# Performance work log

Hardware: AMD Instinct MI355X
Metric: run time of the kernel (lower is better)

The kernel has to match this reference:

```python
import jax, jax.numpy as jnp
import numpy as np

B, C, L = 4, 256, 4096
NUM_GROUPS = 32
EPS = 1e-6


def setup_inputs() -> dict:
    key = jax.random.key(0)
    ks = jax.random.split(key, 8)
    s = 1.0 / np.sqrt(C)  # conv1x1 init scale
    return {
        "x": jax.random.normal(ks[0], (B, C, L), dtype=jnp.float32),
        "norm_g": jnp.ones((C,), dtype=jnp.float32),
        "norm_b": jnp.zeros((C,), dtype=jnp.float32),
        "q_w": jax.random.normal(ks[1], (C, C), dtype=jnp.float32) * s,
        "q_b": jnp.zeros((C,), dtype=jnp.float32),
        "k_w": jax.random.normal(ks[2], (C, C), dtype=jnp.float32) * s,
        "k_b": jnp.zeros((C,), dtype=jnp.float32),
        "v_w": jax.random.normal(ks[3], (C, C), dtype=jnp.float32) * s,
        "v_b": jnp.zeros((C,), dtype=jnp.float32),
        "proj_w": jax.random.normal(ks[4], (C, C), dtype=jnp.float32) * s,
        "proj_b": jnp.zeros((C,), dtype=jnp.float32),
    }


def _group_norm(x, g, b):
    # x: [B, C, L] -> groups of C//NUM_GROUPS channels
    Bx, Cx, Lx = x.shape
    xg = x.reshape(Bx, NUM_GROUPS, Cx // NUM_GROUPS, Lx)
    mean = jnp.mean(xg, axis=(2, 3), keepdims=True)
    var = jnp.var(xg, axis=(2, 3), keepdims=True)
    xn = ((xg - mean) * jax.lax.rsqrt(var + EPS)).reshape(Bx, Cx, Lx)
    return xn * g[None, :, None] + b[None, :, None]


def _conv1x1(w, b, h):
    # w: [Cout, Cin], h: [B, Cin, L]
    return jnp.einsum("oc,bcl->bol", w, h) + b[None, :, None]


def reference(x, norm_g, norm_b, q_w, q_b, k_w, k_b, v_w, v_b, proj_w, proj_b):
    h = _group_norm(x, norm_g, norm_b)
    q = _conv1x1(q_w, q_b, h)   # [B, C, L]
    k = _conv1x1(k_w, k_b, h)
    v = _conv1x1(v_w, v_b, h)

    scale = jnp.asarray(x.shape[1], x.dtype) ** -0.5
    # w_[b,i,j] = sum_c q[b,c,i] * k[b,c,j]
    w_ = jnp.einsum("bci,bcj->bij", q, k) * scale
    w_ = jax.nn.softmax(w_, axis=2)
    # h_[b,c,i] = sum_j v[b,c,j] * w_[b,i,j]
    h2 = jnp.einsum("bcj,bij->bci", v, w_)

    out = _conv1x1(proj_w, proj_b, h2)
    return x + out
```

## Files before the change

### kernel.cpp

```cpp
#include <hip/hip_runtime.h>

#define B_ 4
#define C_ 256
#define L_ 4096
#define NG 32
#define CPG 8
#define BL (B_ * L_)
#define KPART 4
#define KEYS_PP (L_ / KPART)
#define NIT (KEYS_PP / 32)
#define QLOG2E 0.09016844f

typedef __attribute__((ext_vector_type(8))) __bf16 bf16x8;
typedef __attribute__((ext_vector_type(8))) short s16x8;
typedef __attribute__((ext_vector_type(4))) float f32x4;
typedef __attribute__((ext_vector_type(16))) float f32x16;

__device__ __forceinline__ unsigned short f2bf(float f) {
  unsigned int u = __builtin_bit_cast(unsigned int, f);
  u += 0x7fffu + ((u >> 16) & 1u);
  return (unsigned short)(u >> 16);
}
__device__ __forceinline__ float bf2f(unsigned short u) {
  unsigned int v = ((unsigned int)u) << 16;
  return __builtin_bit_cast(float, v);
}
#if __has_builtin(__builtin_amdgcn_exp2f)
#define EXP2F(x) __builtin_amdgcn_exp2f(x)
#else
#define EXP2F(x) exp2f(x)
#endif

__device__ __forceinline__ void gld_lds16(const void* g, void* l) {
  __builtin_amdgcn_global_load_lds(
      (const __attribute__((address_space(1))) unsigned int*)g,
      (__attribute__((address_space(3))) unsigned int*)l, 16, 0, 0);
}

__device__ __forceinline__ float red16_add(float x) {
  int i;
  i = __builtin_amdgcn_update_dpp(0, __builtin_bit_cast(int, x), 0xB1, 0xF, 0xF, false);
  x += __builtin_bit_cast(float, i);
  i = __builtin_amdgcn_update_dpp(0, __builtin_bit_cast(int, x), 0x4E, 0xF, 0xF, false);
  x += __builtin_bit_cast(float, i);
  i = __builtin_amdgcn_update_dpp(0, __builtin_bit_cast(int, x), 0x124, 0xF, 0xF, false);
  x += __builtin_bit_cast(float, i);
  i = __builtin_amdgcn_update_dpp(0, __builtin_bit_cast(int, x), 0x128, 0xF, 0xF, false);
  x += __builtin_bit_cast(float, i);
  return x;
}

__global__ __launch_bounds__(256) void init_k(const float* __restrict__ qw,
                                              const float* __restrict__ kw,
                                              const float* __restrict__ vw,
                                              const float* __restrict__ pw,
                                              const float* __restrict__ qb,
                                              const float* __restrict__ x,
                                              unsigned short* __restrict__ wq,
                                              unsigned short* __restrict__ wk,
                                              unsigned short* __restrict__ wv,
                                              unsigned short* __restrict__ wp,
                                              float* __restrict__ qbs,
                                              float* __restrict__ stats) {
  const int bid = blockIdx.x;
  const int t = threadIdx.x;
  if (bid < 128) {
    const int m = bid >> 5;
    const int blk = bid & 31;
    const float* src = (m == 0) ? qw : (m == 1) ? kw : (m == 2) ? vw : pw;
    unsigned short* dst = (m == 0) ? wq : (m == 1) ? wk : (m == 2) ? wv : wp;
    const float sc = (m == 0) ? QLOG2E : 1.0f;
    const int base = (blk * 256 + t) * 8;
    f32x4 a = *(const f32x4*)(src + base);
    f32x4 b = *(const f32x4*)(src + base + 4);
    s16x8 o;
#pragma unroll
    for (int j = 0; j < 4; ++j) {
      o[j] = (short)f2bf(a[j] * sc);
      o[4 + j] = (short)f2bf(b[j] * sc);
    }
    *(s16x8*)(dst + base) = o;
    if (m == 0 && blk == 0) qbs[t] = qb[t] * QLOG2E;
  } else {
    const int bg = bid - 128;
    const float* base = x + (size_t)bg * (CPG * L_);
    float s = 0.f, ss = 0.f;
#pragma unroll
    for (int i = 0; i < 32; ++i) {
      f32x4 v = *(const f32x4*)(base + (size_t)(t + i * 256) * 4);
#pragma unroll
      for (int j = 0; j < 4; ++j) { s += v[j]; ss += v[j] * v[j]; }
    }
#pragma unroll
    for (int d = 1; d < 64; d <<= 1) {
      s += __shfl_xor(s, d, 64);
      ss += __shfl_xor(ss, d, 64);
    }
    __shared__ float red[8];
    if ((t & 63) == 0) { red[(t >> 6) * 2] = s; red[(t >> 6) * 2 + 1] = ss; }
    __syncthreads();
    if (t == 0) {
      float S = red[0] + red[2] + red[4] + red[6];
      float SS = red[1] + red[3] + red[5] + red[7];
      const float inv_n = 1.f / (float)(CPG * L_);
      float mean = S * inv_n;
      float var = SS * inv_n - mean * mean;
      stats[bg * 2] = mean;
      stats[bg * 2 + 1] = rsqrtf(var + 1e-6f);
    }
  }
}

__global__ __launch_bounds__(256) void gn_apply_k(const float* __restrict__ x,
                                                  const float* __restrict__ stats,
                                                  const float* __restrict__ gam,
                                                  const float* __restrict__ bet,
                                                  unsigned short* __restrict__ ht) {
  __shared__ unsigned short tile[64 * 256];
  const int blk = blockIdx.x;
  const int b = blk >> 6;
  const int l0 = (blk & 63) * 64;
  const int t = threadIdx.x;
  const int c = t;
  const float mean = stats[(b * NG + (c >> 3)) * 2];
  const float rstd = stats[(b * NG + (c >> 3)) * 2 + 1];
  const float sc = rstd * gam[c];
  const float sb = bet[c] - mean * sc;
  const float* row = x + ((size_t)(b * C_ + c)) * L_ + l0;
#pragma unroll
  for (int v = 0; v < 16; ++v) {
    f32x4 f = *(const f32x4*)(row + v * 4);
#pragma unroll
    for (int j = 0; j < 4; ++j) tile[(v * 4 + j) * 256 + c] = f2bf(f[j] * sc + sb);
  }
  __syncthreads();
#pragma unroll
  for (int i = 0; i < 8; ++i) {
    int id = t + i * 256;
    int l = id >> 5, off = id & 31;
    *(s16x8*)(ht + ((size_t)(b * L_) + l0 + l) * 256 + off * 8) =
        *(const s16x8*)(tile + l * 256 + off * 8);
  }
}

__global__ __launch_bounds__(256) void qkv_k(const unsigned short* __restrict__ ht,
                                             const unsigned short* __restrict__ wq,
                                             const unsigned short* __restrict__ wk,
                                             const unsigned short* __restrict__ wv,
                                             const float* __restrict__ qbs,
                                             const float* __restrict__ kbias,
                                             const float* __restrict__ vbias,
                                             unsigned short* __restrict__ qt,
                                             unsigned short* __restrict__ kt,
                                             unsigned short* __restrict__ vg) {
  __shared__ unsigned short Al[64 * 256];
  __shared__ unsigned short Wl[64 * 256];
  const int z = blockIdx.z;
  const unsigned short* W = (z == 0) ? wq : (z == 1) ? wk : wv;
  const float* bias = (z == 0) ? qbs : (z == 1) ? kbias : vbias;
  const int m0 = blockIdx.x * 64;
  const int n0 = blockIdx.y * 64;
  const int t = threadIdx.x;
  const int w = t >> 6, lane = t & 63, l15 = lane & 15, q = lane >> 4;
#pragma unroll
  for (int i = 0; i < 8; ++i) {
    const int seg = w * 8 + i;
    const int idx = seg * 64 + lane;
    const int row = idx >> 5, c16 = idx & 31;
    gld_lds16(ht + (size_t)(m0 + row) * 256 + ((c16 ^ (row & 7)) * 8), Al + seg * 512);
    gld_lds16(W + (size_t)(n0 + row) * 256 + ((c16 ^ (row & 7)) * 8), Wl + seg * 512);
  }
  __syncthreads();
  bf16x8 af[8];
#pragma unroll
  for (int kf = 0; kf < 8; ++kf) {
    int row = w * 16 + l15;
    af[kf] = *(const bf16x8*)(Al + row * 256 + (((kf * 4 + q) ^ (row & 7)) * 8));
  }
  f32x4 acc[4];
#pragma unroll
  for (int nf = 0; nf < 4; ++nf) {
    f32x4 cacc = {0.f, 0.f, 0.f, 0.f};
#pragma unroll
    for (int kf = 0; kf < 8; ++kf) {
      int row = nf * 16 + l15;
      bf16x8 bf = *(const bf16x8*)(Wl + row * 256 + (((kf * 4 + q) ^ (row & 7)) * 8));
      cacc = __builtin_amdgcn_mfma_f32_16x16x32_bf16(af[kf], bf, cacc, 0, 0, 0);
    }
    acc[nf] = cacc;
  }
  unsigned short* Ct = (z == 0) ? qt : kt;
#pragma unroll
  for (int nf = 0; nf < 4; ++nf) {
    const int n = n0 + nf * 16 + l15;
    const float bs = bias[n];
#pragma unroll
    for (int r = 0; r < 4; ++r) {
      const int m = m0 + w * 16 + q * 4 + r;
      const float v = acc[nf][r] + bs;
      if (z < 2) {
        Ct[(size_t)m * 256 + n] = f2bf(v);
      } else {
        const int b = m >> 12, i = m & (L_ - 1);
        const int jt = i >> 5, jj = i & 31;
        const int qc = jj >> 3, pos = jj & 7;
        vg[((size_t)(b * 128 + jt)) * 8192 + n * 32 + ((qc ^ ((n >> 1) & 3)) * 8) + pos] =
            f2bf(v);
      }
    }
  }
}

__global__ __launch_bounds__(256, 2) void attn_k(const unsigned short* __restrict__ Qt,
                                                 const unsigned short* __restrict__ Kt,
                                                 const unsigned short* __restrict__ Vg,
                                                 unsigned short* __restrict__ o0p,
                                                 unsigned short* __restrict__ o1p,
                                                 unsigned short* __restrict__ o2p,
                                                 unsigned short* __restrict__ o3p,
                                                 float* __restrict__ ml) {
  __shared__ unsigned short Kl[2][32 * 256];
  __shared__ unsigned short Vl[2][256 * 32];
  __shared__ unsigned short Pl[4 * 32 * 40];
  const int bid = blockIdx.x;
  const int g = bid & 15;
  const int b = g >> 2, part = g & 3;
  const int qi = bid >> 4;
  const int t = threadIdx.x;
  const int w = t >> 6, lane = t & 63;
  const int l15 = lane & 15, q = lane >> 4;
  const int l31 = lane & 31, h = lane >> 5;

  const int qb0 = b * L_ + qi * 128;
  const int qrow0 = qb0 + w * 32;
  bf16x8 qf[2][8];
#pragma unroll
  for (int mi = 0; mi < 2; ++mi)
#pragma unroll
    for (int kf = 0; kf < 8; ++kf)
      qf[mi][kf] =
          *(const bf16x8*)(Qt + ((size_t)(qrow0 + mi * 16 + l15)) * 256 + kf * 32 + q * 8);

  f32x16 oacc[8];
#pragma unroll
  for (int nf = 0; nf < 8; ++nf)
#pragma unroll
    for (int gg = 0; gg < 16; ++gg) oacc[nf][gg] = 0.f;
  float ls0[4] = {0.f, 0.f, 0.f, 0.f}, ls1[4] = {0.f, 0.f, 0.f, 0.f};

  const unsigned short* kbase = Kt + ((size_t)(b * L_ + part * KEYS_PP)) * 256;
  const unsigned short* vbase = Vg + ((size_t)(b * 128 + part * 32)) * 8192;
  unsigned short* Pw = Pl + w * 1280;

#pragma unroll
  for (int i = 0; i < 4; ++i) {
    const int seg = w * 4 + i;
    const int idx = seg * 64 + lane;
    const int row = idx >> 5, c16 = idx & 31;
    gld_lds16(kbase + (size_t)row * 256 + ((c16 ^ (row & 7)) * 8), &Kl[0][0] + seg * 512);
    gld_lds16(vbase + (size_t)idx * 8, &Vl[0][0] + seg * 512);
  }

  for (int it = 0; it < NIT; ++it) {
    __syncthreads();
    if (it + 1 < NIT) {
      const unsigned short* ksrc = kbase + (size_t)((it + 1) * 32) * 256;
      const unsigned short* vsrc = vbase + (size_t)(it + 1) * 8192;
      unsigned short* kd = &Kl[(it + 1) & 1][0];
      unsigned short* vd = &Vl[(it + 1) & 1][0];
#pragma unroll
      for (int i = 0; i < 4; ++i) {
        const int seg = w * 4 + i;
        const int idx = seg * 64 + lane;
        const int row = idx >> 5, c16 = idx & 31;
        gld_lds16(ksrc + (size_t)row * 256 + ((c16 ^ (row & 7)) * 8), kd + seg * 512);
        gld_lds16(vsrc + (size_t)idx * 8, vd + seg * 512);
      }
    }
    const unsigned short* Kb = &Kl[it & 1][0];
    const unsigned short* Vb = &Vl[it & 1][0];

    f32x4 s00 = {0.f, 0.f, 0.f, 0.f}, s01 = s00, s10 = s00, s11 = s00;
#pragma unroll
    for (int kf = 0; kf < 8; ++kf) {
      const int ch = ((kf * 4 + q) ^ (l15 & 7)) * 8;
      bf16x8 kb0 = *(const bf16x8*)(Kb + l15 * 256 + ch);
      bf16x8 kb1 = *(const bf16x8*)(Kb + (16 + l15) * 256 + ch);
      s00 = __builtin_amdgcn_mfma_f32_16x16x32_bf16(qf[0][kf], kb0, s00, 0, 0, 0);
      s01 = __builtin_amdgcn_mfma_f32_16x16x32_bf16(qf[0][kf], kb1, s01, 0, 0, 0);
      s10 = __builtin_amdgcn_mfma_f32_16x16x32_bf16(qf[1][kf], kb0, s10, 0, 0, 0);
      s11 = __builtin_amdgcn_mfma_f32_16x16x32_bf16(qf[1][kf], kb1, s11, 0, 0, 0);
    }
#pragma unroll
    for (int r = 0; r < 4; ++r) {
      float p00 = EXP2F(s00[r]), p01 = EXP2F(s01[r]);
      float p10 = EXP2F(s10[r]), p11 = EXP2F(s11[r]);
      ls0[r] += p00 + p01;
      ls1[r] += p10 + p11;
      Pw[(q * 4 + r) * 40 + l15] = f2bf(p00);
      Pw[(q * 4 + r) * 40 + 16 + l15] = f2bf(p01);
      Pw[(16 + q * 4 + r) * 40 + l15] = f2bf(p10);
      Pw[(16 + q * 4 + r) * 40 + 16 + l15] = f2bf(p11);
    }
    bf16x8 pa0 = *(const bf16x8*)(Pw + l31 * 40 + h * 8);
    bf16x8 pa1 = *(const bf16x8*)(Pw + l31 * 40 + 16 + h * 8);
#pragma unroll
    for (int nf = 0; nf < 8; ++nf) {
      const int c = nf * 32 + l31;
      bf16x8 v0 = *(const bf16x8*)(Vb + c * 32 + ((h ^ ((c >> 1) & 3)) * 8));
      bf16x8 v1 = *(const bf16x8*)(Vb + c * 32 + (((2 + h) ^ ((c >> 1) & 3)) * 8));
      oacc[nf] = __builtin_amdgcn_mfma_f32_32x32x16_bf16(pa0, v0, oacc[nf], 0, 0, 0);
      oacc[nf] = __builtin_amdgcn_mfma_f32_32x32x16_bf16(pa1, v1, oacc[nf], 0, 0, 0);
    }
  }

  unsigned short* opb = (part == 0) ? o0p : (part == 1) ? o1p : (part == 2) ? o2p : o3p;
#pragma unroll
  for (int nf = 0; nf < 8; ++nf)
#pragma unroll
    for (int gg = 0; gg < 16; ++gg) {
      const int row = (gg & 3) + 8 * (gg >> 2) + 4 * h;
      opb[(size_t)(qrow0 + row) * 256 + nf * 32 + l31] = f2bf(oacc[nf][gg]);
    }
#pragma unroll
  for (int r = 0; r < 4; ++r) {
    ls0[r] = red16_add(ls0[r]);
    ls1[r] = red16_add(ls1[r]);
  }
  if (l15 == 0) {
    float* mlp = ml + (size_t)part * BL;
#pragma unroll
    for (int r = 0; r < 4; ++r) {
      mlp[qrow0 + q * 4 + r] = ls0[r];
      mlp[qrow0 + 16 + q * 4 + r] = ls1[r];
    }
  }
}

__global__ __launch_bounds__(256) void merge_k(const unsigned short* __restrict__ o0p,
                                               const unsigned short* __restrict__ o1p,
                                               const unsigned short* __restrict__ o2p,
                                               const unsigned short* __restrict__ o3p,
                                               const float* __restrict__ ml,
                                               unsigned short* __restrict__ Om) {
  const int row = blockIdx.x * 8 + (threadIdx.x >> 5);
  const int c8 = threadIdx.x & 31;
  const float inv = 1.0f / (ml[row] + ml[BL + row] + ml[2 * BL + row] + ml[3 * BL + row]);
  const size_t off = (size_t)row * 256 + c8 * 8;
  s16x8 v0 = *(const s16x8*)(o0p + off);
  s16x8 v1 = *(const s16x8*)(o1p + off);
  s16x8 v2 = *(const s16x8*)(o2p + off);
  s16x8 v3 = *(const s16x8*)(o3p + off);
  s16x8 o;
#pragma unroll
  for (int j = 0; j < 8; ++j)
    o[j] = (short)f2bf((bf2f((unsigned short)v0[j]) + bf2f((unsigned short)v1[j]) +
                        bf2f((unsigned short)v2[j]) + bf2f((unsigned short)v3[j])) *
                       inv);
  *(s16x8*)(Om + off) = o;
}

__global__ __launch_bounds__(256) void proj_k(const unsigned short* __restrict__ X,
                                              const unsigned short* __restrict__ W,
                                              const float* __restrict__ bias,
                                              const float* __restrict__ xres,
                                              float* __restrict__ out) {
  __shared__ unsigned short Wl[64 * 256];
  __shared__ unsigned short Xl[64 * 256];
  const int i0 = blockIdx.x * 64;
  const int o0 = blockIdx.y * 64;
  const int b = blockIdx.z;
  const int t = threadIdx.x;
  const int w = t >> 6, lane = t & 63, l15 = lane & 15, q = lane >> 4;
#pragma unroll
  for (int i = 0; i < 8; ++i) {
    const int seg = w * 8 + i;
    const int idx = seg * 64 + lane;
    const int row = idx >> 5, c16 = idx & 31;
    gld_lds16(W + (size_t)(o0 + row) * 256 + ((c16 ^ (row & 7)) * 8), Wl + seg * 512);
    gld_lds16(X + ((size_t)(b * L_) + i0 + row) * 256 + ((c16 ^ (row & 7)) * 8),
              Xl + seg * 512);
  }
  __syncthreads();
  bf16x8 af[8];
#pragma unroll
  for (int kf = 0; kf < 8; ++kf) {
    int row = w * 16 + l15;
    af[kf] = *(const bf16x8*)(Wl + row * 256 + (((kf * 4 + q) ^ (row & 7)) * 8));
  }
  f32x4 acc[4];
#pragma unroll
  for (int nf = 0; nf < 4; ++nf) {
    f32x4 cacc = {0.f, 0.f, 0.f, 0.f};
#pragma unroll
    for (int kf = 0; kf < 8; ++kf) {
      int row = nf * 16 + l15;
      bf16x8 bf = *(const bf16x8*)(Xl + row * 256 + (((kf * 4 + q) ^ (row & 7)) * 8));
      cacc = __builtin_amdgcn_mfma_f32_16x16x32_bf16(af[kf], bf, cacc, 0, 0, 0);
    }
    acc[nf] = cacc;
  }
#pragma unroll
  for (int nf = 0; nf < 4; ++nf) {
    const int i = i0 + nf * 16 + l15;
#pragma unroll
    for (int r = 0; r < 4; ++r) {
      const int o = o0 + w * 16 + q * 4 + r;
      const size_t idx = ((size_t)(b * C_ + o)) * L_ + i;
      out[idx] = acc[nf][r] + bias[o] + xres[idx];
    }
  }
}

extern "C" void kernel_launch(void* const* d_in, const int* in_sizes, int n_in,
                              void* d_out, int out_size, void* d_ws, size_t ws_size,
                              hipStream_t stream) {
  const float* x = (const float*)d_in[0];
  const float* norm_g = (const float*)d_in[1];
  const float* norm_b = (const float*)d_in[2];
  const float* q_w = (const float*)d_in[3];
  const float* q_b = (const float*)d_in[4];
  const float* k_w = (const float*)d_in[5];
  const float* k_b = (const float*)d_in[6];
  const float* v_w = (const float*)d_in[7];
  const float* v_b = (const float*)d_in[8];
  const float* p_w = (const float*)d_in[9];
  const float* p_b = (const float*)d_in[10];
  float* out = (float*)d_out;
  (void)in_sizes; (void)n_in; (void)out_size; (void)ws_size;

  char* ws = (char*)d_ws;
  const size_t MB = 1u << 20;
  const size_t PSZ = (size_t)BL * 256 * 2;
  float* stats = (float*)ws;
  float* qbs = (float*)(ws + 1024);
  unsigned short* wq = (unsigned short*)(ws + 4096);
  unsigned short* wk = wq + 65536;
  unsigned short* wv = wk + 65536;
  unsigned short* wp = wv + 65536;
  float* ml = (float*)(ws + 640 * 1024);
  unsigned short* ht = (unsigned short*)(ws + 1 * MB);
  unsigned short* qt = (unsigned short*)(ws + 9 * MB);
  unsigned short* kt = (unsigned short*)(ws + 17 * MB);
  unsigned short* vg = (unsigned short*)(ws + 25 * MB);
  unsigned short* o0p = (unsigned short*)d_out;
  unsigned short* o1p = o0p + PSZ / 2;
  unsigned short* o2p = (unsigned short*)(ws + 33 * MB);
  unsigned short* o3p = o2p + PSZ / 2;

  init_k<<<256, 256, 0, stream>>>(q_w, k_w, v_w, p_w, q_b, x, wq, wk, wv, wp, qbs, stats);
  gn_apply_k<<<B_ * (L_ / 64), 256, 0, stream>>>(x, stats, norm_g, norm_b, ht);
  qkv_k<<<dim3((B_ * L_) / 64, C_ / 64, 3), 256, 0, stream>>>(ht, wq, wk, wv, qbs, k_b,
                                                              v_b, qt, kt, vg);
  attn_k<<<512, 256, 0, stream>>>(qt, kt, vg, o0p, o1p, o2p, o3p, ml);
  merge_k<<<BL / 8, 256, 0, stream>>>(o0p, o1p, o2p, o3p, ml, ht);
  proj_k<<<dim3(L_ / 64, C_ / 64, B_), 256, 0, stream>>>(ht, wp, p_b, x, out);
}
```

Measured before the change: 220.9 us.

## Enlarge QKV GEMM tiles and process 64-key tiles per attention iteration

The QKV projection moves to 128x128 block tiles with a two-step K loop, so each wave computes a 64x64 sub-tile with more operand reuse. The attention kernel now loads 64 keys per iteration with a new V layout grouped in 8-key chunks, and drops the K/V double buffering in favour of load-then-compute with two barriers. The P staging pitch is reduced. Global load latency in attention is no longer overlapped with compute, and the narrower P pitch may cause LDS bank conflicts or misaligned vector reads.

```diff
diff --git a/kernel.cpp b/kernel.cpp
--- a/kernel.cpp
+++ b/kernel.cpp
@@ -8,7 +8,7 @@
 #define BL (B_ * L_)
 #define KPART 4
 #define KEYS_PP (L_ / KPART)
-#define NIT (KEYS_PP / 32)
+#define NIT (KEYS_PP / 64)
 #define QLOG2E 0.09016844f
 
 typedef __attribute__((ext_vector_type(8))) __bf16 bf16x8;
@@ -143,69 +143,85 @@
   }
 }
 
-__global__ __launch_bounds__(256) void qkv_k(const unsigned short* __restrict__ ht,
-                                             const unsigned short* __restrict__ wq,
-                                             const unsigned short* __restrict__ wk,
-                                             const unsigned short* __restrict__ wv,
-                                             const float* __restrict__ qbs,
-                                             const float* __restrict__ kbias,
-                                             const float* __restrict__ vbias,
-                                             unsigned short* __restrict__ qt,
-                                             unsigned short* __restrict__ kt,
-                                             unsigned short* __restrict__ vg) {
-  __shared__ unsigned short Al[64 * 256];
-  __shared__ unsigned short Wl[64 * 256];
+__global__ __launch_bounds__(256, 2) void qkv_k(const unsigned short* __restrict__ ht,
+                                                const unsigned short* __restrict__ wq,
+                                                const unsigned short* __restrict__ wk,
+                                                const unsigned short* __restrict__ wv,
+                                                const float* __restrict__ qbs,
+                                                const float* __restrict__ kbias,
+                                                const float* __restrict__ vbias,
+                                                unsigned short* __restrict__ qt,
+                                                unsigned short* __restrict__ kt,
+                                                unsigned short* __restrict__ vg) {
+  __shared__ unsigned short Al[128 * 128];
+  __shared__ unsigned short Wl[128 * 128];
   const int z = blockIdx.z;
   const unsigned short* W = (z == 0) ? wq : (z == 1) ? wk : wv;
   const float* bias = (z == 0) ? qbs : (z == 1) ? kbias : vbias;
-  const int m0 = blockIdx.x * 64;
-  const int n0 = blockIdx.y * 64;
+  const int m0 = blockIdx.x * 128;
+  const int n0 = blockIdx.y * 128;
   const int t = threadIdx.x;
   const int w = t >> 6, lane = t & 63, l15 = lane & 15, q = lane >> 4;
-#pragma unroll
-  for (int i = 0; i < 8; ++i) {
-    const int seg = w * 8 + i;
-    const int idx = seg * 64 + lane;
-    const int row = idx >> 5, c16 = idx & 31;
-    gld_lds16(ht + (size_t)(m0 + row) * 256 + ((c16 ^ (row & 7)) * 8), Al + seg * 512);
-    gld_lds16(W + (size_t)(n0 + row) * 256 + ((c16 ^ (row & 7)) * 8), Wl + seg * 512);
-  }
-  __syncthreads();
-  bf16x8 af[8];
-#pragma unroll
-  for (int kf = 0; kf < 8; ++kf) {
-    int row = w * 16 + l15;
-    af[kf] = *(const bf16x8*)(Al + row * 256 + (((kf * 4 + q) ^ (row & 7)) * 8));
-  }
-  f32x4 acc[4];
-#pragma unroll
-  for (int nf = 0; nf < 4; ++nf) {
-    f32x4 cacc = {0.f, 0.f, 0.f, 0.f};
-#pragma unroll
-    for (int kf = 0; kf < 8; ++kf) {
-      int row = nf * 16 + l15;
-      bf16x8 bf = *(const bf16x8*)(Wl + row * 256 + (((kf * 4 + q) ^ (row & 7)) * 8));
-      cacc = __builtin_amdgcn_mfma_f32_16x16x32_bf16(af[kf], bf, cacc, 0, 0, 0);
-    }
-    acc[nf] = cacc;
+  const int mw = (w & 1) * 64, nw = (w >> 1) * 64;
+
+  f32x4 acc[4][4];
+#pragma unroll
+  for (int mi = 0; mi < 4; ++mi)
+#pragma unroll
+    for (int ni = 0; ni < 4; ++ni) acc[mi][ni] = {0.f, 0.f, 0.f, 0.f};
+
+  for (int k0 = 0; k0 < 256; k0 += 128) {
+    __syncthreads();
+#pragma unroll
+    for (int i = 0; i < 8; ++i) {
+      const int seg = w * 8 + i;
+      const int idx = seg * 64 + lane;
+      const int row = idx >> 4, c16 = idx & 15;
+      const int gch = (c16 ^ (row & 15)) * 8;
+      gld_lds16(ht + (size_t)(m0 + row) * 256 + k0 + gch, Al + seg * 512);
+      gld_lds16(W + (size_t)(n0 + row) * 256 + k0 + gch, Wl + seg * 512);
+    }
+    __syncthreads();
+#pragma unroll
+    for (int ks = 0; ks < 4; ++ks) {
+      bf16x8 af[4], bf[4];
+#pragma unroll
+      for (int mi = 0; mi < 4; ++mi) {
+        const int row = mw + mi * 16 + l15;
+        af[mi] = *(const bf16x8*)(Al + row * 128 + (((ks * 4 + q) ^ (row & 15)) * 8));
+      }
+#pragma unroll
+      for (int ni = 0; ni < 4; ++ni) {
+        const int row = nw + ni * 16 + l15;
+        bf[ni] = *(const bf16x8*)(Wl + row * 128 + (((ks * 4 + q) ^ (row & 15)) * 8));
+      }
+#pragma unroll
+      for (int mi = 0; mi < 4; ++mi)
+#pragma unroll
+        for (int ni = 0; ni < 4; ++ni)
+          acc[mi][ni] =
+              __builtin_amdgcn_mfma_f32_16x16x32_bf16(af[mi], bf[ni], acc[mi][ni], 0, 0, 0);
+    }
   }
   unsigned short* Ct = (z == 0) ? qt : kt;
 #pragma unroll
-  for (int nf = 0; nf < 4; ++nf) {
-    const int n = n0 + nf * 16 + l15;
+  for (int ni = 0; ni < 4; ++ni) {
+    const int n = n0 + nw + ni * 16 + l15;
     const float bs = bias[n];
 #pragma unroll
-    for (int r = 0; r < 4; ++r) {
-      const int m = m0 + w * 16 + q * 4 + r;
-      const float v = acc[nf][r] + bs;
-      if (z < 2) {
-        Ct[(size_t)m * 256 + n] = f2bf(v);
-      } else {
-        const int b = m >> 12, i = m & (L_ - 1);
-        const int jt = i >> 5, jj = i & 31;
-        const int qc = jj >> 3, pos = jj & 7;
-        vg[((size_t)(b * 128 + jt)) * 8192 + n * 32 + ((qc ^ ((n >> 1) & 3)) * 8) + pos] =
-            f2bf(v);
+    for (int mi = 0; mi < 4; ++mi) {
+#pragma unroll
+      for (int r = 0; r < 4; ++r) {
+        const int m = m0 + mw + mi * 16 + q * 4 + r;
+        const float v = acc[mi][ni][r] + bs;
+        if (z < 2) {
+          Ct[(size_t)m * 256 + n] = f2bf(v);
+        } else {
+          const int b = m >> 12, i = m & (L_ - 1);
+          const int jt = i >> 6, j = i & 63;
+          vg[((size_t)(b * 64 + jt)) * 16384 + ((j >> 3) * 256 + n) * 8 + (j & 7)] =
+              f2bf(v);
+        }
       }
     }
   }
@@ -219,9 +235,9 @@
                                                  unsigned short* __restrict__ o2p,
                                                  unsigned short* __restrict__ o3p,
                                                  float* __restrict__ ml) {
-  __shared__ unsigned short Kl[2][32 * 256];
-  __shared__ unsigned short Vl[2][256 * 32];
-  __shared__ unsigned short Pl[4 * 32 * 40];
+  __shared__ unsigned short Kl[64 * 256];
+  __shared__ unsigned short Vl[8 * 256 * 8];
+  __shared__ unsigned short Pl[4 * 32 * 20];
   const int bid = blockIdx.x;
   const int g = bid & 15;
   const int b = g >> 2, part = g & 3;
@@ -249,68 +265,50 @@
   float ls0[4] = {0.f, 0.f, 0.f, 0.f}, ls1[4] = {0.f, 0.f, 0.f, 0.f};
 
   const unsigned short* kbase = Kt + ((size_t)(b * L_ + part * KEYS_PP)) * 256;
-  const unsigned short* vbase = Vg + ((size_t)(b * 128 + part * 32)) * 8192;
-  unsigned short* Pw = Pl + w * 1280;
-
-#pragma unroll
-  for (int i = 0; i < 4; ++i) {
-    const int seg = w * 4 + i;
-    const int idx = seg * 64 + lane;
-    const int row = idx >> 5, c16 = idx & 31;
-    gld_lds16(kbase + (size_t)row * 256 + ((c16 ^ (row & 7)) * 8), &Kl[0][0] + seg * 512);
-    gld_lds16(vbase + (size_t)idx * 8, &Vl[0][0] + seg * 512);
-  }
+  const unsigned short* vbase = Vg + ((size_t)(b * 64 + part * 16)) * 16384;
+  unsigned short* Pw = Pl + w * 640;
 
   for (int it = 0; it < NIT; ++it) {
     __syncthreads();
-    if (it + 1 < NIT) {
-      const unsigned short* ksrc = kbase + (size_t)((it + 1) * 32) * 256;
-      const unsigned short* vsrc = vbase + (size_t)(it + 1) * 8192;
-      unsigned short* kd = &Kl[(it + 1) & 1][0];
-      unsigned short* vd = &Vl[(it + 1) & 1][0];
-#pragma unroll
-      for (int i = 0; i < 4; ++i) {
-        const int seg = w * 4 + i;
+    {
+      const unsigned short* ksrc = kbase + (size_t)(it * 64) * 256;
+      const unsigned short* vsrc = vbase + (size_t)it * 16384;
+#pragma unroll
+      for (int i = 0; i < 8; ++i) {
+        const int seg = w * 8 + i;
         const int idx = seg * 64 + lane;
         const int row = idx >> 5, c16 = idx & 31;
-        gld_lds16(ksrc + (size_t)row * 256 + ((c16 ^ (row & 7)) * 8), kd + seg * 512);
-        gld_lds16(vsrc + (size_t)idx * 8, vd + seg * 512);
-      }
-    }
-    const unsigned short* Kb = &Kl[it & 1][0];
-    const unsigned short* Vb = &Vl[it & 1][0];
-
-    f32x4 s00 = {0.f, 0.f, 0.f, 0.f}, s01 = s00, s10 = s00, s11 = s00;
-#pragma unroll
-    for (int kf = 0; kf < 8; ++kf) {
-      const int ch = ((kf * 4 + q) ^ (l15 & 7)) * 8;
-      bf16x8 kb0 = *(const bf16x8*)(Kb + l15 * 256 + ch);
-      bf16x8 kb1 = *(const bf16x8*)(Kb + (16 + l15) * 256 + ch);
-      s00 = __builtin_amdgcn_mfma_f32_16x16x32_bf16(qf[0][kf], kb0, s00, 0, 0, 0);
-      s01 = __builtin_amdgcn_mfma_f32_16x16x32_bf16(qf[0][kf], kb1, s01, 0, 0, 0);
-      s10 = __builtin_amdgcn_mfma_f32_16x16x32_bf16(qf[1][kf], kb0, s10, 0, 0, 0);
-      s11 = __builtin_amdgcn_mfma_f32_16x16x32_bf16(qf[1][kf], kb1, s11, 0, 0, 0);
-    }
-#pragma unroll
-    for (int r = 0; r < 4; ++r) {
-      float p00 = EXP2F(s00[r]), p01 = EXP2F(s01[r]);
-      float p10 = EXP2F(s10[r]), p11 = EXP2F(s11[r]);
-      ls0[r] += p00 + p01;
-      ls1[r] += p10 + p11;
-      Pw[(q * 4 + r) * 40 + l15] = f2bf(p00);
-      Pw[(q * 4 + r) * 40 + 16 + l15] = f2bf(p01);
-      Pw[(16 + q * 4 + r) * 40 + l15] = f2bf(p10);
-      Pw[(16 + q * 4 + r) * 40 + 16 + l15] = f2bf(p11);
-    }
-    bf16x8 pa0 = *(const bf16x8*)(Pw + l31 * 40 + h * 8);
-    bf16x8 pa1 = *(const bf16x8*)(Pw + l31 * 40 + 16 + h * 8);
-#pragma unroll
-    for (int nf = 0; nf < 8; ++nf) {
-      const int c = nf * 32 + l31;
-      bf16x8 v0 = *(const bf16x8*)(Vb + c * 32 + ((h ^ ((c >> 1) & 3)) * 8));
-      bf16x8 v1 = *(const bf16x8*)(Vb + c * 32 + (((2 + h) ^ ((c >> 1) & 3)) * 8));
-      oacc[nf] = __builtin_amdgcn_mfma_f32_32x32x16_bf16(pa0, v0, oacc[nf], 0, 0, 0);
-      oacc[nf] = __builtin_amdgcn_mfma_f32_32x32x16_bf16(pa1, v1, oacc[nf], 0, 0, 0);
+        gld_lds16(ksrc + (size_t)row * 256 + ((c16 ^ (row & 7)) * 8), Kl + seg * 512);
+        gld_lds16(vsrc + (size_t)idx * 8, Vl + seg * 512);
+      }
+    }
+    __syncthreads();
+
+#pragma unroll
+    for (int kc = 0; kc < 4; ++kc) {
+      f32x4 s0 = {0.f, 0.f, 0.f, 0.f}, s1 = s0;
+#pragma unroll
+      for (int kf = 0; kf < 8; ++kf) {
+        const int row = kc * 16 + l15;
+        bf16x8 kb = *(const bf16x8*)(Kl + row * 256 + (((kf * 4 + q) ^ (row & 7)) * 8));
+        s0 = __builtin_amdgcn_mfma_f32_16x16x32_bf16(qf[0][kf], kb, s0, 0, 0, 0);
+        s1 = __builtin_amdgcn_mfma_f32_16x16x32_bf16(qf[1][kf], kb, s1, 0, 0, 0);
+      }
+#pragma unroll
+      for (int r = 0; r < 4; ++r) {
+        float p0 = EXP2F(s0[r]), p1 = EXP2F(s1[r]);
+        ls0[r] += p0;
+        ls1[r] += p1;
+        Pw[(q * 4 + r) * 20 + l15] = f2bf(p0);
+        Pw[(16 + q * 4 + r) * 20 + l15] = f2bf(p1);
+      }
+      bf16x8 pa = *(const bf16x8*)(Pw + l31 * 20 + h * 8);
+#pragma unroll
+      for (int nf = 0; nf < 8; ++nf) {
+        bf16x8 vv =
+            *(const bf16x8*)(Vl + ((kc * 2 + h) * 256 + nf * 32 + l31) * 8);
+        oacc[nf] = __builtin_amdgcn_mfma_f32_32x32x16_bf16(pa, vv, oacc[nf], 0, 0, 0);
+      }
     }
   }
 
@@ -450,8 +448,8 @@
 
   init_k<<<256, 256, 0, stream>>>(q_w, k_w, v_w, p_w, q_b, x, wq, wk, wv, wp, qbs, stats);
   gn_apply_k<<<B_ * (L_ / 64), 256, 0, stream>>>(x, stats, norm_g, norm_b, ht);
-  qkv_k<<<dim3((B_ * L_) / 64, C_ / 64, 3), 256, 0, stream>>>(ht, wq, wk, wv, qbs, k_b,
-                                                              v_b, qt, kt, vg);
+  qkv_k<<<dim3(BL / 128, C_ / 128, 3), 256, 0, stream>>>(ht, wq, wk, wv, qbs, k_b, v_b,
+                                                         qt, kt, vg);
   attn_k<<<512, 256, 0, stream>>>(qt, kt, vg, o0p, o1p, o2p, o3p, ml);
   merge_k<<<BL / 8, 256, 0, stream>>>(o0p, o1p, o2p, o3p, ml, ht);
   proj_k<<<dim3(L_ / 64, C_ / 64, B_), 256, 0, stream>>>(ht, wp, p_b, x, out);
```

Measured after the change: 248.0 us. 1.12x slower.
